# Performance work log

Hardware: AMD Instinct MI355X
Metric: run time of the kernel (lower is better)

## Reference

```python
import jax, jax.numpy as jnp
import numpy as np

D = 256   # input_dim (also per-head dim)
H = 8     # num_heads
B = 32
S = 1024


def setup_inputs() -> dict:
    key = jax.random.key(0)
    ks = jax.random.split(key, 9)
    scale = 1.0 / np.sqrt(D)
    x = jax.random.normal(ks[0], (B, S, D), dtype=jnp.float32)
    Wk = jax.random.normal(ks[1], (D, D * H), dtype=jnp.float32) * scale
    bk = jnp.zeros((D * H,), dtype=jnp.float32)
    Wv = jax.random.normal(ks[2], (D, D * H), dtype=jnp.float32) * scale
    bv = jnp.zeros((D * H,), dtype=jnp.float32)
    query = jax.random.normal(ks[3], (H, D), dtype=jnp.float32)
    Wo = jax.random.normal(ks[4], (D * H, D), dtype=jnp.float32) / np.sqrt(D * H)
    bo = jnp.zeros((D,), dtype=jnp.float32)
    return {"x": x, "Wk": Wk, "bk": bk, "Wv": Wv, "bv": bv,
            "query": query, "Wo": Wo, "bo": bo}


def reference(x, Wk, bk, Wv, bv, query, Wo, bo):
    b, s, _ = x.shape
    # keys/values: [B, S, H, D]
    keys = (x @ Wk + bk).reshape(b, s, H, D)
    values = (x @ Wv + bv).reshape(b, s, H, D)
    # per-head single-query scores over sequence: [B, S, H]
    scores = jnp.einsum("bshd,hd->bsh", keys, query)
    attn = jax.nn.softmax(scores, axis=1)
    # attention-pooled values per head: [B, H, D] -> concat [B, H*D]
    pooled = jnp.einsum("bsh,bshd->bhd", attn, values).reshape(b, H * D)
    return pooled @ Wo + bo
```

## Files before the change

kernel.cpp:

```cpp
#include <hip/hip_runtime.h>

#define D 256
#define H 8
#define B 32
#define S 1024
#define SCH 16
#define SCS 64

#define OFF_QK     0
#define OFF_SB     2048
#define OFF_ML     2056
#define OFF_XWP    10248
#define OFF_POOLED 1058824

__global__ void k_prep(const float* __restrict__ Wk, const float* __restrict__ bk,
                       const float* __restrict__ query, const float* __restrict__ bo,
                       float* __restrict__ qk, float* __restrict__ sb,
                       float* __restrict__ out) {
    const int h  = blockIdx.x >> 3;
    const int kc = blockIdx.x & 7;
    const int t  = threadIdx.x;
    __shared__ float qsh[D];
    __shared__ float red[D];
    qsh[t] = query[h * D + t];
    __syncthreads();
    const int kl = t >> 3;
    const int dq = t & 7;
    const int k  = kc * 32 + kl;
    const float* wrow = Wk + (size_t)k * (D * H) + h * D;
    float acc = 0.f;
    #pragma unroll
    for (int i = 0; i < 8; i++) {
        const int d = i * 32 + dq * 4;
        const float4 w = *(const float4*)(wrow + d);
        acc += w.x * qsh[d] + w.y * qsh[d + 1] + w.z * qsh[d + 2] + w.w * qsh[d + 3];
    }
    acc += __shfl_xor(acc, 1);
    acc += __shfl_xor(acc, 2);
    acc += __shfl_xor(acc, 4);
    if (dq == 0) qk[h * D + k] = acc;
    if (kc == 0) {
        red[t] = bk[h * D + t] * qsh[t];
        __syncthreads();
        for (int st = 128; st > 0; st >>= 1) {
            if (t < st) red[t] += red[t + st];
            __syncthreads();
        }
        if (t == 0) sb[h] = red[0];
    }
    if (h == 0) {
        const float bov = bo[t];
        #pragma unroll
        for (int bb = 0; bb < 4; bb++)
            out[(size_t)(kc * 4 + bb) * D + t] = bov;
    }
}

__global__ void k_fused(const float* __restrict__ x, const float* __restrict__ qk,
                        const float* __restrict__ sb, float* __restrict__ xwp,
                        float2* __restrict__ mlbuf) {
    const int b  = blockIdx.x >> 4;
    const int c  = blockIdx.x & 15;
    const int s0 = c * SCS;
    const int t  = threadIdx.x;
    __shared__ float qkL[H * D];
    __shared__ float sc[SCS][H];
    #pragma unroll
    for (int i = 0; i < 8; i++) qkL[i * 256 + t] = qk[i * 256 + t];
    __syncthreads();

    {
        const int sl = t >> 2;
        const int dq = t & 3;
        const int d0 = dq * 64;
        float accA[H] = {};
        const float* xrow = x + ((size_t)(b * S + s0 + sl)) * D + d0;
        #pragma unroll 4
        for (int i = 0; i < 16; i++) {
            const float4 xv = *(const float4*)(xrow + i * 4);
            #pragma unroll
            for (int hh = 0; hh < H; hh++) {
                const float4 qv = *(const float4*)(&qkL[hh * D + d0 + i * 4]);
                accA[hh] += xv.x * qv.x + xv.y * qv.y + xv.z * qv.z + xv.w * qv.w;
            }
        }
        #pragma unroll
        for (int hh = 0; hh < H; hh++) {
            accA[hh] += __shfl_xor(accA[hh], 1);
            accA[hh] += __shfl_xor(accA[hh], 2);
        }
        if (dq == 0) {
            #pragma unroll
            for (int hh = 0; hh < H; hh++)
                sc[sl][hh] = accA[hh] + sb[hh];
        }
    }
    __syncthreads();

    {
        const int hh = t >> 5;
        const int u  = t & 31;
        const float v0 = sc[u][hh], v1 = sc[u + 32][hh];
        float m = fmaxf(v0, v1);
        #pragma unroll
        for (int msk = 1; msk < 32; msk <<= 1) m = fmaxf(m, __shfl_xor(m, msk));
        const float e0 = __expf(v0 - m), e1 = __expf(v1 - m);
        float sum = e0 + e1;
        #pragma unroll
        for (int msk = 1; msk < 32; msk <<= 1) sum += __shfl_xor(sum, msk);
        sc[u][hh] = e0;
        sc[u + 32][hh] = e1;
        if (u == 0) mlbuf[((size_t)(b * SCH + c)) * H + hh] = make_float2(m, sum);
    }
    __syncthreads();

    {
        float acc2[H] = {};
        const float* xp = x + ((size_t)(b * S + s0)) * D + t;
        for (int s = 0; s < SCS; s++) {
            const float xv = xp[(size_t)s * D];
            const float4 pa = *(const float4*)(&sc[s][0]);
            const float4 pb = *(const float4*)(&sc[s][4]);
            acc2[0] += pa.x * xv; acc2[1] += pa.y * xv;
            acc2[2] += pa.z * xv; acc2[3] += pa.w * xv;
            acc2[4] += pb.x * xv; acc2[5] += pb.y * xv;
            acc2[6] += pb.z * xv; acc2[7] += pb.w * xv;
        }
        #pragma unroll
        for (int hh = 0; hh < H; hh++)
            xwp[(((size_t)(b * SCH + c)) * H + hh) * D + t] = acc2[hh];
    }
}

__global__ void k_pooled(const float* __restrict__ xwp, const float2* __restrict__ mlbuf,
                         const float* __restrict__ Wv, const float* __restrict__ bv,
                         float* __restrict__ pooled) {
    const int bh = blockIdx.x;
    const int b = bh >> 3, h = bh & 7;
    const int j = threadIdx.x;
    __shared__ float xwL[D];
    __shared__ float scaleL[SCH];
    __shared__ float2 mlL[SCH];
    if (j < SCH) mlL[j] = mlbuf[((size_t)(b * SCH + j)) * H + h];
    __syncthreads();
    if (j == 0) {
        float M = -1e30f;
        for (int cc = 0; cc < SCH; cc++) M = fmaxf(M, mlL[cc].x);
        float L = 0.f;
        for (int cc = 0; cc < SCH; cc++) L += mlL[cc].y * __expf(mlL[cc].x - M);
        const float invL = 1.f / L;
        for (int cc = 0; cc < SCH; cc++) scaleL[cc] = __expf(mlL[cc].x - M) * invL;
    }
    __syncthreads();
    float acc = 0.f;
    #pragma unroll
    for (int cc = 0; cc < SCH; cc++)
        acc += xwp[(((size_t)(b * SCH + cc)) * H + h) * D + j] * scaleL[cc];
    xwL[j] = acc;
    __syncthreads();
    const float* wcol = Wv + h * D + j;
    float a2 = 0.f;
    #pragma unroll 8
    for (int d = 0; d < D; d++)
        a2 += xwL[d] * wcol[(size_t)d * (D * H)];
    pooled[(size_t)b * (D * H) + h * D + j] = a2 + bv[h * D + j];
}

__global__ void k_out(const float* __restrict__ pooled, const float* __restrict__ Wo,
                      float* __restrict__ out) {
    const int b  = blockIdx.x >> 3;
    const int kc = blockIdx.x & 7;
    const int j  = threadIdx.x;
    __shared__ float pL[256];
    pL[j] = pooled[(size_t)b * (D * H) + kc * 256 + j];
    __syncthreads();
    const float* wp = Wo + (size_t)(kc * 256) * D + j;
    float acc = 0.f;
    #pragma unroll 8
    for (int cc = 0; cc < 256; cc++)
        acc += pL[cc] * wp[(size_t)cc * D];
    atomicAdd(out + (size_t)b * D + j, acc);
}

extern "C" void kernel_launch(void* const* d_in, const int* in_sizes, int n_in,
                              void* d_out, int out_size, void* d_ws, size_t ws_size,
                              hipStream_t stream) {
    const float* x     = (const float*)d_in[0];
    const float* Wk    = (const float*)d_in[1];
    const float* bk    = (const float*)d_in[2];
    const float* Wv    = (const float*)d_in[3];
    const float* bv    = (const float*)d_in[4];
    const float* query = (const float*)d_in[5];
    const float* Wo    = (const float*)d_in[6];
    const float* bo    = (const float*)d_in[7];
    float* out = (float*)d_out;
    float* ws  = (float*)d_ws;

    float*  qk     = ws + OFF_QK;
    float*  sb     = ws + OFF_SB;
    float2* mlbuf  = (float2*)(ws + OFF_ML);
    float*  xwp    = ws + OFF_XWP;
    float*  pooled = ws + OFF_POOLED;

    k_prep<<<dim3(H * 8), dim3(256), 0, stream>>>(Wk, bk, query, bo, qk, sb, out);
    k_fused<<<dim3(B * SCH), dim3(256), 0, stream>>>(x, qk, sb, xwp, mlbuf);
    k_pooled<<<dim3(B * H), dim3(256), 0, stream>>>(xwp, mlbuf, Wv, bv, pooled);
    k_out<<<dim3(B * 8), dim3(256), 0, stream>>>(pooled, Wo, out);
}
```

Baseline: 127.7 us.

## Split sequence into more chunks and widen per-row parallelism in score kernel

After: 128.6 us. No clear change (+0.7%).

```diff
diff --git a/kernel.cpp b/kernel.cpp
--- a/kernel.cpp
+++ b/kernel.cpp
@@ -4,43 +4,40 @@
 #define H 8
 #define B 32
 #define S 1024
-#define SCH 16
-#define SCS 64
+#define SCH 32
+#define SCS 32
 
 #define OFF_QK     0
 #define OFF_SB     2048
 #define OFF_ML     2056
-#define OFF_XWP    10248
-#define OFF_POOLED 1058824
+#define OFF_XWP    18440
+#define OFF_POOLED 2115592
 
 __global__ void k_prep(const float* __restrict__ Wk, const float* __restrict__ bk,
                        const float* __restrict__ query, const float* __restrict__ bo,
                        float* __restrict__ qk, float* __restrict__ sb,
                        float* __restrict__ out) {
-    const int h  = blockIdx.x >> 3;
-    const int kc = blockIdx.x & 7;
+    __shared__ float red[256];
+    const int h  = blockIdx.x >> 5;
+    const int kc = blockIdx.x & 31;
     const int t  = threadIdx.x;
-    __shared__ float qsh[D];
-    __shared__ float red[D];
-    qsh[t] = query[h * D + t];
-    __syncthreads();
-    const int kl = t >> 3;
-    const int dq = t & 7;
-    const int k  = kc * 32 + kl;
-    const float* wrow = Wk + (size_t)k * (D * H) + h * D;
-    float acc = 0.f;
+    const int kl = t >> 5;
+    const int dq = t & 31;
+    const int k  = kc * 8 + kl;
+    const int d0 = dq * 8;
+    const float* wrow = Wk + (size_t)k * (D * H) + h * D + d0;
+    const float* qrow = query + h * D + d0;
+    const float4 w0 = *(const float4*)(wrow);
+    const float4 w1 = *(const float4*)(wrow + 4);
+    const float4 q0 = *(const float4*)(qrow);
+    const float4 q1 = *(const float4*)(qrow + 4);
+    float acc = w0.x * q0.x + w0.y * q0.y + w0.z * q0.z + w0.w * q0.w
+              + w1.x * q1.x + w1.y * q1.y + w1.z * q1.z + w1.w * q1.w;
     #pragma unroll
-    for (int i = 0; i < 8; i++) {
-        const int d = i * 32 + dq * 4;
-        const float4 w = *(const float4*)(wrow + d);
-        acc += w.x * qsh[d] + w.y * qsh[d + 1] + w.z * qsh[d + 2] + w.w * qsh[d + 3];
-    }
-    acc += __shfl_xor(acc, 1);
-    acc += __shfl_xor(acc, 2);
-    acc += __shfl_xor(acc, 4);
+    for (int msk = 1; msk < 32; msk <<= 1) acc += __shfl_xor(acc, msk);
     if (dq == 0) qk[h * D + k] = acc;
     if (kc == 0) {
-        red[t] = bk[h * D + t] * qsh[t];
+        red[t] = bk[h * D + t] * query[h * D + t];
         __syncthreads();
         for (int st = 128; st > 0; st >>= 1) {
             if (t < st) red[t] += red[t + st];
@@ -48,39 +45,46 @@
         }
         if (t == 0) sb[h] = red[0];
     }
-    if (h == 0) {
-        const float bov = bo[t];
-        #pragma unroll
-        for (int bb = 0; bb < 4; bb++)
-            out[(size_t)(kc * 4 + bb) * D + t] = bov;
-    }
+    if (h == 0) out[(size_t)kc * D + t] = bo[t];
 }
 
 __global__ void k_fused(const float* __restrict__ x, const float* __restrict__ qk,
                         const float* __restrict__ sb, float* __restrict__ xwp,
                         float2* __restrict__ mlbuf) {
-    const int b  = blockIdx.x >> 4;
-    const int c  = blockIdx.x & 15;
+    const int b  = blockIdx.x >> 5;
+    const int c  = blockIdx.x & 31;
     const int s0 = c * SCS;
     const int t  = threadIdx.x;
     __shared__ float qkL[H * D];
+    __shared__ float sbL[H];
     __shared__ float sc[SCS][H];
-    #pragma unroll
-    for (int i = 0; i < 8; i++) qkL[i * 256 + t] = qk[i * 256 + t];
-    __syncthreads();
-
-    {
-        const int sl = t >> 2;
-        const int dq = t & 3;
-        const int d0 = dq * 64;
+    {
+        float4* q4 = (float4*)qkL;
+        q4[t]       = ((const float4*)qk)[t];
+        q4[t + 256] = ((const float4*)qk)[t + 256];
+        if (t < H) sbL[t] = sb[t];
+    }
+    __syncthreads();
+
+    {
+        const int sl = t >> 3;
+        const int dq = t & 7;
+        const int d0 = dq * 32;
+        const float* xrow = x + ((size_t)(b * S + s0 + sl)) * D + d0;
+        float4 xr[8];
+        #pragma unroll
+        for (int j0 = 0; j0 < 8; j0++) {
+            const int j = (j0 + dq) & 7;
+            xr[j0] = *(const float4*)(xrow + j * 4);
+        }
         float accA[H] = {};
-        const float* xrow = x + ((size_t)(b * S + s0 + sl)) * D + d0;
-        #pragma unroll 4
-        for (int i = 0; i < 16; i++) {
-            const float4 xv = *(const float4*)(xrow + i * 4);
+        #pragma unroll
+        for (int j0 = 0; j0 < 8; j0++) {
+            const int j = (j0 + dq) & 7;
+            const float4 xv = xr[j0];
             #pragma unroll
             for (int hh = 0; hh < H; hh++) {
-                const float4 qv = *(const float4*)(&qkL[hh * D + d0 + i * 4]);
+                const float4 qv = *(const float4*)(&qkL[hh * D + d0 + j * 4]);
                 accA[hh] += xv.x * qv.x + xv.y * qv.y + xv.z * qv.z + xv.w * qv.w;
             }
         }
@@ -88,11 +92,12 @@
         for (int hh = 0; hh < H; hh++) {
             accA[hh] += __shfl_xor(accA[hh], 1);
             accA[hh] += __shfl_xor(accA[hh], 2);
+            accA[hh] += __shfl_xor(accA[hh], 4);
         }
         if (dq == 0) {
             #pragma unroll
             for (int hh = 0; hh < H; hh++)
-                sc[sl][hh] = accA[hh] + sb[hh];
+                sc[sl][hh] = accA[hh] + sbL[hh];
         }
     }
     __syncthreads();
@@ -100,16 +105,15 @@
     {
         const int hh = t >> 5;
         const int u  = t & 31;
-        const float v0 = sc[u][hh], v1 = sc[u + 32][hh];
-        float m = fmaxf(v0, v1);
+        const float v = sc[u][hh];
+        float m = v;
         #pragma unroll
         for (int msk = 1; msk < 32; msk <<= 1) m = fmaxf(m, __shfl_xor(m, msk));
-        const float e0 = __expf(v0 - m), e1 = __expf(v1 - m);
-        float sum = e0 + e1;
+        const float e = __expf(v - m);
+        float sum = e;
         #pragma unroll
         for (int msk = 1; msk < 32; msk <<= 1) sum += __shfl_xor(sum, msk);
-        sc[u][hh] = e0;
-        sc[u + 32][hh] = e1;
+        sc[u][hh] = e;
         if (u == 0) mlbuf[((size_t)(b * SCH + c)) * H + hh] = make_float2(m, sum);
     }
     __syncthreads();
@@ -117,6 +121,7 @@
     {
         float acc2[H] = {};
         const float* xp = x + ((size_t)(b * S + s0)) * D + t;
+        #pragma unroll 4
         for (int s = 0; s < SCS; s++) {
             const float xv = xp[(size_t)s * D];
             const float4 pa = *(const float4*)(&sc[s][0]);
@@ -202,7 +207,7 @@
     float*  xwp    = ws + OFF_XWP;
     float*  pooled = ws + OFF_POOLED;
 
-    k_prep<<<dim3(H * 8), dim3(256), 0, stream>>>(Wk, bk, query, bo, qk, sb, out);
+    k_prep<<<dim3(H * 32), dim3(256), 0, stream>>>(Wk, bk, query, bo, qk, sb, out);
     k_fused<<<dim3(B * SCH), dim3(256), 0, stream>>>(x, qk, sb, xwp, mlbuf);
     k_pooled<<<dim3(B * H), dim3(256), 0, stream>>>(xwp, mlbuf, Wv, bv, pooled);
     k_out<<<dim3(B * 8), dim3(256), 0, stream>>>(pooled, Wo, out);
```
